# Optimization experiments

Measured on AMD Instinct MI355X. Metric: run time of the kernel, lower is better.

Reference implementation:

```python
import jax, jax.numpy as jnp
import numpy as np
import math

B, S, E, NH = 1024, 16, 32, 4  # batch, seq, attn embed dim, heads
H = 64                          # lstm1 hidden; lstm2 hidden = H//2 = E


def _pos_encoding(s, d):
    pos = jnp.arange(s, dtype=jnp.float32)[:, None]
    div = jnp.exp(jnp.arange(0, d, 2, dtype=jnp.float32) * (-math.log(10000.0) / d))
    pe = jnp.zeros((s, d), jnp.float32)
    pe = pe.at[:, 0::2].set(jnp.sin(pos * div))
    pe = pe.at[:, 1::2].set(jnp.cos(pos * div))
    return pe


def _lstm(x, wih, whh, bih, bhh):
    # x: [B,S,in]; PyTorch gate order i,f,g,o; h0=c0=0
    b = x.shape[0]
    h_dim = whh.shape[1]
    xg = jnp.einsum('bsi,gi->bsg', x, wih) + bih + bhh  # precompute input contribution

    def step(carry, xt):
        h, c = carry
        g = xt + h @ whh.T
        i, f, gg, o = jnp.split(g, 4, axis=-1)
        c = jax.nn.sigmoid(f) * c + jax.nn.sigmoid(i) * jnp.tanh(gg)
        h = jax.nn.sigmoid(o) * jnp.tanh(c)
        return (h, c), h

    h0 = jnp.zeros((b, h_dim), x.dtype)
    _, hs = jax.lax.scan(step, (h0, h0), jnp.swapaxes(xg, 0, 1))
    return jnp.swapaxes(hs, 0, 1)  # [B,S,H]


def setup_inputs() -> dict:
    key = jax.random.key(0)
    ks = jax.random.split(key, 24)

    def rn(k, shape, s=0.15):
        return jax.random.normal(k, shape, jnp.float32) * s

    return {
        'x': jax.random.normal(ks[0], (B, S, 1), jnp.float32),
        'emb_w': rn(ks[1], (32, 1)), 'emb_b': rn(ks[2], (32,), 0.05),
        'l1_wih': rn(ks[3], (4 * H, 32)), 'l1_whh': rn(ks[4], (4 * H, H)),
        'l1_bih': rn(ks[5], (4 * H,), 0.05), 'l1_bhh': rn(ks[6], (4 * H,), 0.05),
        'l2_wih': rn(ks[7], (4 * (H // 2), H)), 'l2_whh': rn(ks[8], (4 * (H // 2), H // 2)),
        'l2_bih': rn(ks[9], (4 * (H // 2),), 0.05), 'l2_bhh': rn(ks[10], (4 * (H // 2),), 0.05),
        'attn_w': rn(ks[11], (3 * E, E)), 'attn_b': rn(ks[12], (3 * E,), 0.05),
        'attn_ow': rn(ks[13], (E, E)), 'attn_ob': rn(ks[14], (E,), 0.05),
        'd1_w': rn(ks[15], (64, E)), 'd1_b': rn(ks[16], (64,), 0.05),
        'bn1_g': jnp.ones((64,), jnp.float32), 'bn1_b': jnp.zeros((64,), jnp.float32),
        'd2_w': rn(ks[17], (32, 64)), 'd2_b': rn(ks[18], (32,), 0.05),
        'bn2_g': jnp.ones((32,), jnp.float32), 'bn2_b': jnp.zeros((32,), jnp.float32),
        'd3_w': rn(ks[19], (1, 32)), 'd3_b': rn(ks[20], (1,), 0.05),
    }


def reference(x, emb_w, emb_b, l1_wih, l1_whh, l1_bih, l1_bhh,
              l2_wih, l2_whh, l2_bih, l2_bhh,
              attn_w, attn_b, attn_ow, attn_ob,
              d1_w, d1_b, bn1_g, bn1_b, d2_w, d2_b, bn2_g, bn2_b, d3_w, d3_b):
    eps = 1e-5
    h = x @ emb_w.T + emb_b                      # [B,S,32]
    h = h + _pos_encoding(h.shape[1], h.shape[2])
    l1 = _lstm(h, l1_wih, l1_whh, l1_bih, l1_bhh)          # [B,S,64]  (dropout: eval -> id)
    l2 = _lstm(l1, l2_wih, l2_whh, l2_bih, l2_bhh)         # [B,S,32]
    l2 = l2 + l1[:, :, :l2.shape[2]]                        # residual

    # nn.MultiheadAttention with default batch_first=False: attends over axis 0 (=B here),
    # faithful to the original module's behavior.
    L, N, _ = l2.shape
    hd = E // NH
    qkv = l2 @ attn_w.T + attn_b
    q, k, v = jnp.split(qkv, 3, axis=-1)
    q = q.reshape(L, N, NH, hd) * (1.0 / math.sqrt(hd))
    k = k.reshape(L, N, NH, hd)
    v = v.reshape(L, N, NH, hd)
    scores = jnp.einsum('lnhd,mnhd->nhlm', q, k)           # [S,4,B,B]
    a = jax.nn.softmax(scores, axis=-1)
    att = jnp.einsum('nhlm,mnhd->lnhd', a, v).reshape(L, N, E)
    att = att @ attn_ow.T + attn_ob

    z = att[:, -1, :]                                       # [B,32]

    def bn(t, g, b):  # eval-mode BatchNorm1d with fresh running stats (mean=0, var=1)
        return t * (g / jnp.sqrt(1.0 + eps)) + b

    z = jax.nn.relu(bn(z @ d1_w.T + d1_b, bn1_g, bn1_b))
    z = jax.nn.relu(bn(z @ d2_w.T + d2_b, bn2_g, bn2_b))
    return jax.nn.sigmoid(z @ d3_w.T + d3_b)                # [B,1]
```

## Files before the change

### kernel.cpp

```cpp
#include <hip/hip_runtime.h>
#include <math.h>


typedef __attribute__((ext_vector_type(8))) short short8v;
typedef __attribute__((ext_vector_type(4))) float f32x4;

__device__ __forceinline__ float sigf(float x) { return 1.0f / (1.0f + __expf(-x)); }
__device__ __forceinline__ float tanh_f(float x) {
    float a = fabsf(x);
    float e = __expf(2.0f * a);
    float t = 1.0f - 2.0f / (e + 1.0f);
    return copysignf(t, x);
}
__device__ __forceinline__ unsigned short f2bf(float f) {
    unsigned int u = __float_as_uint(f);
    unsigned int r = (u + 0x7FFFu + ((u >> 16) & 1u)) >> 16;
    return (unsigned short)r;
}

__global__ __launch_bounds__(256, 1) void lstm_kernel(
    const float* __restrict__ x,
    const float* __restrict__ emb_w, const float* __restrict__ emb_b,
    const float* __restrict__ wih1, const float* __restrict__ whh1,
    const float* __restrict__ bih1, const float* __restrict__ bhh1,
    const float* __restrict__ wih2, const float* __restrict__ whh2,
    const float* __restrict__ bih2, const float* __restrict__ bhh2,
    const float* __restrict__ attn_w, const float* __restrict__ attn_b,
    float* __restrict__ Q, float* __restrict__ K, float* __restrict__ V) {
    const int tid = threadIdx.x;
    const int w = tid >> 6, lane = tid & 63;
    const int l15 = lane & 15, q4 = lane >> 4;
    const int base = blockIdx.x * 16;

    __shared__ __align__(16) unsigned char E_raw[16 * 1024];
    __shared__ __align__(16) unsigned char H1_raw[2][2048];
    __shared__ __align__(16) unsigned char H2_raw[2][1024];
    __shared__ __align__(16) unsigned char WF2[24 * 1024];
    __shared__ __align__(16) float L1F[16][64];
    __shared__ __align__(16) float L2F[16][32];

    const unsigned jx7 = (unsigned)(l15 & 7) << 4;
    const unsigned jx4 = (unsigned)(l15 & 3) << 4;

    short8v w1f[4][3];
#pragma unroll
    for (int t = 0; t < 4; t++) {
        const int row = (w + 4 * t) * 16 + l15;
#pragma unroll
        for (int sl = 0; sl < 3; sl++) {
            short8v f;
#pragma unroll
            for (int e = 0; e < 8; e++) {
                int k = sl * 32 + q4 * 8 + e;
                float v = (k < 64) ? whh1[row * 64 + k] : wih1[row * 32 + (k - 64)];
                f[e] = (short)f2bf(v);
            }
            w1f[t][sl] = f;
        }
    }

    for (int f = w; f < 24; f += 4) {
        int t2 = f / 3, sl = f - t2 * 3;
        int row = t2 * 16 + l15;
        int koff = sl * 32 + q4 * 8;
        const float* src = (sl < 2) ? (wih2 + row * 64 + koff) : (whh2 + row * 32 + (koff - 64));
        float4 va = *(const float4*)(src);
        float4 vb = *(const float4*)(src + 4);
        short8v pk;
        pk[0] = (short)f2bf(va.x); pk[1] = (short)f2bf(va.y);
        pk[2] = (short)f2bf(va.z); pk[3] = (short)f2bf(va.w);
        pk[4] = (short)f2bf(vb.x); pk[5] = (short)f2bf(vb.y);
        pk[6] = (short)f2bf(vb.z); pk[7] = (short)f2bf(vb.w);
        *(short8v*)(&WF2[f * 1024 + lane * 16]) = pk;
    }

    float b1r[4][4];
#pragma unroll
    for (int t = 0; t < 4; t++)
#pragma unroll
        for (int e = 0; e < 4; e++) {
            int r = (w + 4 * t) * 16 + q4 * 4 + e;
            b1r[t][e] = bih1[r] + bhh1[r];
        }
    float b2r[4][4];
#pragma unroll
    for (int t = 0; t < 4; t++)
#pragma unroll
        for (int e = 0; e < 4; e++) {
            int r = ((w & 1) + 2 * t) * 16 + q4 * 4 + e;
            b2r[t][e] = bih2[r] + bhh2[r];
        }

    *(unsigned long long*)(H1_raw[0] + tid * 8) = 0ULL;
    if (tid < 128) *(unsigned long long*)(H2_raw[0] + tid * 8) = 0ULL;
    {
        const int je = tid >> 4, se = tid & 15;
        float xv = x[(base + je) * 16 + se];
        float ev[32];
#pragma unroll
        for (int ii = 0; ii < 16; ii++) {
            float d = __expf(-0.28782313662425574f * (float)(2 * ii));
            float ang = (float)se * d;
            ev[2 * ii] = xv * emb_w[2 * ii] + emb_b[2 * ii] + __sinf(ang);
            ev[2 * ii + 1] = xv * emb_w[2 * ii + 1] + emb_b[2 * ii + 1] + __cosf(ang);
        }
        unsigned jm = (unsigned)(je & 3) << 4;
#pragma unroll
        for (int b = 0; b < 4; b++) {
            short8v pk;
#pragma unroll
            for (int e = 0; e < 8; e++) pk[e] = (short)f2bf(ev[b * 8 + e]);
            *(short8v*)(&E_raw[se * 1024 + je * 64 + (((unsigned)(b * 16)) ^ jm)]) = pk;
        }
    }
    float c1[4] = {0.f, 0.f, 0.f, 0.f};
    float c2[4] = {0.f, 0.f, 0.f, 0.f};
    __syncthreads();

    const int u0 = w * 16 + q4 * 4;
    const int u20 = w * 16 + q4 * 4;

#define L2FRAG(T, SL) (*(const short8v*)(&WF2[(((w + 2 * (T)) * 3 + (SL)) << 10) + lane * 16]))

#pragma unroll 2
    for (int s = 0; s < 16; s++) {
        const int p = s & 1, pn = p ^ 1;
        const unsigned char* H1p = H1_raw[p];
        unsigned char* H1n = H1_raw[pn];
        short8v B0 = *(const short8v*)(H1p + (((unsigned)(l15 * 128 + q4 * 16)) ^ jx7));
        short8v B1 = *(const short8v*)(H1p + (((unsigned)(l15 * 128 + 64 + q4 * 16)) ^ jx7));
        short8v BE = *(const short8v*)(&E_raw[s * 1024] + (((unsigned)(l15 * 64 + q4 * 16)) ^ jx4));
        f32x4 a0 = {b1r[0][0], b1r[0][1], b1r[0][2], b1r[0][3]};
        f32x4 a1 = {b1r[1][0], b1r[1][1], b1r[1][2], b1r[1][3]};
        f32x4 a2 = {b1r[2][0], b1r[2][1], b1r[2][2], b1r[2][3]};
        f32x4 a3 = {b1r[3][0], b1r[3][1], b1r[3][2], b1r[3][3]};
        a0 = __builtin_amdgcn_mfma_f32_16x16x32_bf16(w1f[0][0], B0, a0, 0, 0, 0);
        a1 = __builtin_amdgcn_mfma_f32_16x16x32_bf16(w1f[1][0], B0, a1, 0, 0, 0);
        a2 = __builtin_amdgcn_mfma_f32_16x16x32_bf16(w1f[2][0], B0, a2, 0, 0, 0);
        a3 = __builtin_amdgcn_mfma_f32_16x16x32_bf16(w1f[3][0], B0, a3, 0, 0, 0);
        a0 = __builtin_amdgcn_mfma_f32_16x16x32_bf16(w1f[0][1], B1, a0, 0, 0, 0);
        a1 = __builtin_amdgcn_mfma_f32_16x16x32_bf16(w1f[1][1], B1, a1, 0, 0, 0);
        a2 = __builtin_amdgcn_mfma_f32_16x16x32_bf16(w1f[2][1], B1, a2, 0, 0, 0);
        a3 = __builtin_amdgcn_mfma_f32_16x16x32_bf16(w1f[3][1], B1, a3, 0, 0, 0);
        a0 = __builtin_amdgcn_mfma_f32_16x16x32_bf16(w1f[0][2], BE, a0, 0, 0, 0);
        a1 = __builtin_amdgcn_mfma_f32_16x16x32_bf16(w1f[1][2], BE, a1, 0, 0, 0);
        a2 = __builtin_amdgcn_mfma_f32_16x16x32_bf16(w1f[2][2], BE, a2, 0, 0, 0);
        a3 = __builtin_amdgcn_mfma_f32_16x16x32_bf16(w1f[3][2], BE, a3, 0, 0, 0);
        float h1v[4];
#pragma unroll
        for (int e = 0; e < 4; e++) {
            c1[e] = sigf(a1[e]) * c1[e] + sigf(a0[e]) * tanh_f(a2[e]);
            h1v[e] = sigf(a3[e]) * tanh_f(c1[e]);
        }
        {
            unsigned long long pk =
                (unsigned long long)f2bf(h1v[0]) | ((unsigned long long)f2bf(h1v[1]) << 16) |
                ((unsigned long long)f2bf(h1v[2]) << 32) | ((unsigned long long)f2bf(h1v[3]) << 48);
            *(unsigned long long*)(H1n + (((unsigned)(l15 * 128 + u0 * 2)) ^ jx7)) = pk;
        }
        if (s == 15) *(float4*)(&L1F[l15][u0]) = make_float4(h1v[0], h1v[1], h1v[2], h1v[3]);
        __syncthreads();
        if (w < 2) {
            const unsigned char* H2p = H2_raw[p];
            short8v C0 = *(const short8v*)(H1n + (((unsigned)(l15 * 128 + q4 * 16)) ^ jx7));
            short8v C1f = *(const short8v*)(H1n + (((unsigned)(l15 * 128 + 64 + q4 * 16)) ^ jx7));
            short8v C2 = *(const short8v*)(H2p + (((unsigned)(l15 * 64 + q4 * 16)) ^ jx4));
            f32x4 d0 = {b2r[0][0], b2r[0][1], b2r[0][2], b2r[0][3]};
            f32x4 d1 = {b2r[1][0], b2r[1][1], b2r[1][2], b2r[1][3]};
            f32x4 d2 = {b2r[2][0], b2r[2][1], b2r[2][2], b2r[2][3]};
            f32x4 d3 = {b2r[3][0], b2r[3][1], b2r[3][2], b2r[3][3]};
            d0 = __builtin_amdgcn_mfma_f32_16x16x32_bf16(L2FRAG(0, 0), C0, d0, 0, 0, 0);
            d1 = __builtin_amdgcn_mfma_f32_16x16x32_bf16(L2FRAG(1, 0), C0, d1, 0, 0, 0);
            d2 = __builtin_amdgcn_mfma_f32_16x16x32_bf16(L2FRAG(2, 0), C0, d2, 0, 0, 0);
            d3 = __builtin_amdgcn_mfma_f32_16x16x32_bf16(L2FRAG(3, 0), C0, d3, 0, 0, 0);
            d0 = __builtin_amdgcn_mfma_f32_16x16x32_bf16(L2FRAG(0, 1), C1f, d0, 0, 0, 0);
            d1 = __builtin_amdgcn_mfma_f32_16x16x32_bf16(L2FRAG(1, 1), C1f, d1, 0, 0, 0);
            d2 = __builtin_amdgcn_mfma_f32_16x16x32_bf16(L2FRAG(2, 1), C1f, d2, 0, 0, 0);
            d3 = __builtin_amdgcn_mfma_f32_16x16x32_bf16(L2FRAG(3, 1), C1f, d3, 0, 0, 0);
            d0 = __builtin_amdgcn_mfma_f32_16x16x32_bf16(L2FRAG(0, 2), C2, d0, 0, 0, 0);
            d1 = __builtin_amdgcn_mfma_f32_16x16x32_bf16(L2FRAG(1, 2), C2, d1, 0, 0, 0);
            d2 = __builtin_amdgcn_mfma_f32_16x16x32_bf16(L2FRAG(2, 2), C2, d2, 0, 0, 0);
            d3 = __builtin_amdgcn_mfma_f32_16x16x32_bf16(L2FRAG(3, 2), C2, d3, 0, 0, 0);
            float h2v[4];
#pragma unroll
            for (int e = 0; e < 4; e++) {
                c2[e] = sigf(d1[e]) * c2[e] + sigf(d0[e]) * tanh_f(d2[e]);
                h2v[e] = sigf(d3[e]) * tanh_f(c2[e]);
            }
            unsigned long long pk =
                (unsigned long long)f2bf(h2v[0]) | ((unsigned long long)f2bf(h2v[1]) << 16) |
                ((unsigned long long)f2bf(h2v[2]) << 32) | ((unsigned long long)f2bf(h2v[3]) << 48);
            *(unsigned long long*)(H2_raw[pn] + (((unsigned)(l15 * 64 + u20 * 2)) ^ jx4)) = pk;
            if (s == 15) *(float4*)(&L2F[l15][u20]) = make_float4(h2v[0], h2v[1], h2v[2], h2v[3]);
        }
        __syncthreads();
    }

    {
        const int j = tid >> 4, rb = tid & 15;
        const int gb = base + j;
        const float4* l1p = (const float4*)(&L1F[j][0]);
        const float4* l2p = (const float4*)(&L2F[j][0]);
#pragma unroll
        for (int rep = 0; rep < 6; rep++) {
            int row = rb + 16 * rep;
            float acc = attn_b[row];
            const float4* wrow = (const float4*)(attn_w + row * 32);
#pragma unroll
            for (int k4 = 0; k4 < 8; k4++) {
                float4 lv1 = l1p[k4];
                float4 lv2 = l2p[k4];
                float4 ww = wrow[k4];
                float lx = lv2.x + lv1.x, ly = lv2.y + lv1.y, lz = lv2.z + lv1.z, lw = lv2.w + lv1.w;
                acc += lx * ww.x + ly * ww.y + lz * ww.z + lw * ww.w;
            }
            if (row < 32) Q[gb * 32 + row] = acc * 0.35355339059327373f;
            else if (row < 64) K[gb * 32 + (row - 32)] = acc;
            else V[gb * 32 + (row - 64)] = acc;
        }
    }
#undef L2FRAG
}

__global__ __launch_bounds__(256, 2) void attn_kernel(
    const float* __restrict__ Q, const float* __restrict__ K, const float* __restrict__ V,
    float* __restrict__ pm, float* __restrict__ ps, float* __restrict__ pacc) {
    int c = blockIdx.x & 15, lt = blockIdx.x >> 4;
    int t = threadIdx.x;
    int h = t >> 6, l = lt * 64 + (t & 63);
    __shared__ __align__(16) float Ks[64 * 32];
    __shared__ __align__(16) float Vs[64 * 32];
    {
        const float4* Kg = (const float4*)(K + c * 2048);
        const float4* Vg = (const float4*)(V + c * 2048);
        float4* K4 = (float4*)Ks;
        float4* V4 = (float4*)Vs;
        K4[t] = Kg[t];
        K4[t + 256] = Kg[t + 256];
        V4[t] = Vg[t];
        V4[t + 256] = Vg[t + 256];
    }
    const float4* qg = (const float4*)(Q + l * 32 + h * 8);
    float4 q0 = qg[0], q1 = qg[1];
    __syncthreads();
    float m_r = -1e30f, l_r = 0.f;
    float4 acc0 = {0, 0, 0, 0}, acc1 = {0, 0, 0, 0};
#pragma unroll 4
    for (int m = 0; m < 64; m++) {
        const float4* k4 = (const float4*)(Ks + m * 32 + h * 8);
        float4 ka = k4[0], kb = k4[1];
        float s = q0.x * ka.x + q0.y * ka.y + q0.z * ka.z + q0.w * ka.w +
                  q1.x * kb.x + q1.y * kb.y + q1.z * kb.z + q1.w * kb.w;
        const float4* v4 = (const float4*)(Vs + m * 32 + h * 8);
        float4 va = v4[0], vb = v4[1];
        float nm = fmaxf(m_r, s);
        float f = __expf(m_r - nm);
        float pp = __expf(s - nm);
        l_r = l_r * f + pp;
        acc0.x = acc0.x * f + pp * va.x;
        acc0.y = acc0.y * f + pp * va.y;
        acc0.z = acc0.z * f + pp * va.z;
        acc0.w = acc0.w * f + pp * va.w;
        acc1.x = acc1.x * f + pp * vb.x;
        acc1.y = acc1.y * f + pp * vb.y;
        acc1.z = acc1.z * f + pp * vb.z;
        acc1.w = acc1.w * f + pp * vb.w;
        m_r = nm;
    }
    int idx = (c * 4 + h) * 1024 + l;
    pm[idx] = m_r;
    ps[idx] = l_r;
    float4* po = (float4*)(pacc + idx * 8);
    po[0] = acc0;
    po[1] = acc1;
}

__global__ __launch_bounds__(256) void head_kernel(
    const float* __restrict__ pm, const float* __restrict__ ps, const float* __restrict__ pacc,
    const float* __restrict__ ow, const float* __restrict__ ob,
    const float* __restrict__ d1w, const float* __restrict__ d1b,
    const float* __restrict__ g1, const float* __restrict__ b1,
    const float* __restrict__ d2w, const float* __restrict__ d2b,
    const float* __restrict__ g2, const float* __restrict__ b2,
    const float* __restrict__ d3w, const float* __restrict__ d3b,
    float* __restrict__ out) {
    int wid = threadIdx.x >> 6, j = threadIdx.x & 63;
    int l = blockIdx.x * 4 + wid;
    __shared__ float att_s[4][32], z_s[4][32], r1s[4][64];
    if (j < 32) {
        int h = j >> 3, d = j & 7;
        float M = -1e30f;
#pragma unroll
        for (int c = 0; c < 16; c++) M = fmaxf(M, pm[(c * 4 + h) * 1024 + l]);
        float den = 0.f, num = 0.f;
#pragma unroll
        for (int c = 0; c < 16; c++) {
            int idx = (c * 4 + h) * 1024 + l;
            float e = __expf(pm[idx] - M);
            den += e * ps[idx];
            num += e * pacc[idx * 8 + d];
        }
        att_s[wid][j] = num / den;
    }
    __syncthreads();
    if (j < 32) {
        float a = ob[j];
#pragma unroll
        for (int i = 0; i < 32; i++) a += att_s[wid][i] * ow[j * 32 + i];
        z_s[wid][j] = a;
    }
    __syncthreads();
    const float inv = rsqrtf(1.0f + 1e-5f);
    if (j < 64) {
        float a = d1b[j];
#pragma unroll
        for (int i = 0; i < 32; i++) a += z_s[wid][i] * d1w[j * 32 + i];
        a = a * (g1[j] * inv) + b1[j];
        r1s[wid][j] = fmaxf(a, 0.f);
    }
    __syncthreads();
    if (j < 32) {
        float a = d2b[j];
#pragma unroll
        for (int i = 0; i < 64; i++) a += r1s[wid][i] * d2w[j * 64 + i];
        a = a * (g2[j] * inv) + b2[j];
        float r2 = fmaxf(a, 0.f);
        float p = r2 * d3w[j];
        p += __shfl_down(p, 16);
        p += __shfl_down(p, 8);
        p += __shfl_down(p, 4);
        p += __shfl_down(p, 2);
        p += __shfl_down(p, 1);
        if (j == 0) out[l] = 1.0f / (1.0f + __expf(-(p + d3b[0])));
    }
}

extern "C" void kernel_launch(void* const* d_in, const int* in_sizes, int n_in,
                              void* d_out, int out_size, void* d_ws, size_t ws_size,
                              hipStream_t stream) {
    const float* x      = (const float*)d_in[0];
    const float* emb_w  = (const float*)d_in[1];
    const float* emb_b  = (const float*)d_in[2];
    const float* l1_wih = (const float*)d_in[3];
    const float* l1_whh = (const float*)d_in[4];
    const float* l1_bih = (const float*)d_in[5];
    const float* l1_bhh = (const float*)d_in[6];
    const float* l2_wih = (const float*)d_in[7];
    const float* l2_whh = (const float*)d_in[8];
    const float* l2_bih = (const float*)d_in[9];
    const float* l2_bhh = (const float*)d_in[10];
    const float* attn_w = (const float*)d_in[11];
    const float* attn_b = (const float*)d_in[12];
    const float* attn_ow = (const float*)d_in[13];
    const float* attn_ob = (const float*)d_in[14];
    const float* d1_w  = (const float*)d_in[15];
    const float* d1_b  = (const float*)d_in[16];
    const float* bn1_g = (const float*)d_in[17];
    const float* bn1_b = (const float*)d_in[18];
    const float* d2_w  = (const float*)d_in[19];
    const float* d2_b  = (const float*)d_in[20];
    const float* bn2_g = (const float*)d_in[21];
    const float* bn2_b = (const float*)d_in[22];
    const float* d3_w  = (const float*)d_in[23];
    const float* d3_b  = (const float*)d_in[24];
    float* out = (float*)d_out;

    float* ws   = (float*)d_ws;
    float* Q    = ws;
    float* K    = ws + 32768;
    float* V    = ws + 65536;
    float* pm   = ws + 98304;
    float* ps   = ws + 163840;
    float* pacc = ws + 229376;

    lstm_kernel<<<64, 256, 0, stream>>>(x, emb_w, emb_b, l1_wih, l1_whh, l1_bih, l1_bhh,
                                        l2_wih, l2_whh, l2_bih, l2_bhh,
                                        attn_w, attn_b, Q, K, V);
    attn_kernel<<<256, 256, 0, stream>>>(Q, K, V, pm, ps, pacc);
    head_kernel<<<256, 256, 0, stream>>>(pm, ps, pacc, attn_ow, attn_ob, d1_w, d1_b,
                                         bn1_g, bn1_b, d2_w, d2_b, bn2_g, bn2_b,
                                         d3_w, d3_b, out);
}
```

Before: 162.5 us.

## Software-pipeline LSTM layers to halve barriers per step and use fast rcp/bf16 packing

Restructures the LSTM recurrence so layer-1 step s+1 runs after layer-2 step s within the same barrier interval. The two layers now share the H1 fragment loads, and the second __syncthreads per timestep goes away. The sigmoid and tanh divisions become hardware reciprocals, and bf16 packing uses v_cvt_pk_bf16_f32. The dense head loops in the attention-combine kernel are vectorized with float4. Risks are small precision differences from the approximate reciprocal and subtle correctness issues in the reordered double-buffer indexing.

```diff
diff --git a/kernel.cpp b/kernel.cpp
--- a/kernel.cpp
+++ b/kernel.cpp
@@ -5,17 +5,25 @@
 typedef __attribute__((ext_vector_type(8))) short short8v;
 typedef __attribute__((ext_vector_type(4))) float f32x4;
 
-__device__ __forceinline__ float sigf(float x) { return 1.0f / (1.0f + __expf(-x)); }
+__device__ __forceinline__ float sigf(float x) {
+    float e = __expf(-x);
+    return __builtin_amdgcn_rcpf(1.0f + e);
+}
 __device__ __forceinline__ float tanh_f(float x) {
     float a = fabsf(x);
     float e = __expf(2.0f * a);
-    float t = 1.0f - 2.0f / (e + 1.0f);
+    float t = 1.0f - 2.0f * __builtin_amdgcn_rcpf(e + 1.0f);
     return copysignf(t, x);
 }
 __device__ __forceinline__ unsigned short f2bf(float f) {
     unsigned int u = __float_as_uint(f);
     unsigned int r = (u + 0x7FFFu + ((u >> 16) & 1u)) >> 16;
     return (unsigned short)r;
+}
+__device__ __forceinline__ unsigned cvtpk_bf16(float lo, float hi) {
+    unsigned r;
+    asm("v_cvt_pk_bf16_f32 %0, %1, %2" : "=v"(r) : "v"(lo), "v"(hi));
+    return r;
 }
 
 __global__ __launch_bounds__(256, 1) void lstm_kernel(
@@ -91,8 +99,8 @@
             b2r[t][e] = bih2[r] + bhh2[r];
         }
 
-    *(unsigned long long*)(H1_raw[0] + tid * 8) = 0ULL;
-    if (tid < 128) *(unsigned long long*)(H2_raw[0] + tid * 8) = 0ULL;
+    *(unsigned long long*)(H1_raw[1] + tid * 8) = 0ULL;
+    if (tid < 128) *(unsigned long long*)(H2_raw[1] + tid * 8) = 0ULL;
     {
         const int je = tid >> 4, se = tid & 15;
         float xv = x[(base + je) * 16 + se];
@@ -115,25 +123,24 @@
     }
     float c1[4] = {0.f, 0.f, 0.f, 0.f};
     float c2[4] = {0.f, 0.f, 0.f, 0.f};
-    __syncthreads();
 
     const int u0 = w * 16 + q4 * 4;
-    const int u20 = w * 16 + q4 * 4;
-
+
+#define LDBE(S)  (*(const short8v*)(&E_raw[(S) * 1024] + (((unsigned)(l15 * 64 + q4 * 16)) ^ jx4)))
+#define LDB0(HP) (*(const short8v*)((HP) + (((unsigned)(l15 * 128 + q4 * 16)) ^ jx7)))
+#define LDB1(HP) (*(const short8v*)((HP) + (((unsigned)(l15 * 128 + 64 + q4 * 16)) ^ jx7)))
+#define LDC2(HP) (*(const short8v*)((HP) + (((unsigned)(l15 * 64 + q4 * 16)) ^ jx4)))
 #define L2FRAG(T, SL) (*(const short8v*)(&WF2[(((w + 2 * (T)) * 3 + (SL)) << 10) + lane * 16]))
 
-#pragma unroll 2
-    for (int s = 0; s < 16; s++) {
-        const int p = s & 1, pn = p ^ 1;
-        const unsigned char* H1p = H1_raw[p];
-        unsigned char* H1n = H1_raw[pn];
-        short8v B0 = *(const short8v*)(H1p + (((unsigned)(l15 * 128 + q4 * 16)) ^ jx7));
-        short8v B1 = *(const short8v*)(H1p + (((unsigned)(l15 * 128 + 64 + q4 * 16)) ^ jx7));
-        short8v BE = *(const short8v*)(&E_raw[s * 1024] + (((unsigned)(l15 * 64 + q4 * 16)) ^ jx4));
+    auto phase1 = [&](unsigned char* H1n, short8v BE, short8v B0, short8v B1, bool last) {
         f32x4 a0 = {b1r[0][0], b1r[0][1], b1r[0][2], b1r[0][3]};
         f32x4 a1 = {b1r[1][0], b1r[1][1], b1r[1][2], b1r[1][3]};
         f32x4 a2 = {b1r[2][0], b1r[2][1], b1r[2][2], b1r[2][3]};
         f32x4 a3 = {b1r[3][0], b1r[3][1], b1r[3][2], b1r[3][3]};
+        a0 = __builtin_amdgcn_mfma_f32_16x16x32_bf16(w1f[0][2], BE, a0, 0, 0, 0);
+        a1 = __builtin_amdgcn_mfma_f32_16x16x32_bf16(w1f[1][2], BE, a1, 0, 0, 0);
+        a2 = __builtin_amdgcn_mfma_f32_16x16x32_bf16(w1f[2][2], BE, a2, 0, 0, 0);
+        a3 = __builtin_amdgcn_mfma_f32_16x16x32_bf16(w1f[3][2], BE, a3, 0, 0, 0);
         a0 = __builtin_amdgcn_mfma_f32_16x16x32_bf16(w1f[0][0], B0, a0, 0, 0, 0);
         a1 = __builtin_amdgcn_mfma_f32_16x16x32_bf16(w1f[1][0], B0, a1, 0, 0, 0);
         a2 = __builtin_amdgcn_mfma_f32_16x16x32_bf16(w1f[2][0], B0, a2, 0, 0, 0);
@@ -142,41 +149,41 @@
         a1 = __builtin_amdgcn_mfma_f32_16x16x32_bf16(w1f[1][1], B1, a1, 0, 0, 0);
         a2 = __builtin_amdgcn_mfma_f32_16x16x32_bf16(w1f[2][1], B1, a2, 0, 0, 0);
         a3 = __builtin_amdgcn_mfma_f32_16x16x32_bf16(w1f[3][1], B1, a3, 0, 0, 0);
-        a0 = __builtin_amdgcn_mfma_f32_16x16x32_bf16(w1f[0][2], BE, a0, 0, 0, 0);
-        a1 = __builtin_amdgcn_mfma_f32_16x16x32_bf16(w1f[1][2], BE, a1, 0, 0, 0);
-        a2 = __builtin_amdgcn_mfma_f32_16x16x32_bf16(w1f[2][2], BE, a2, 0, 0, 0);
-        a3 = __builtin_amdgcn_mfma_f32_16x16x32_bf16(w1f[3][2], BE, a3, 0, 0, 0);
         float h1v[4];
 #pragma unroll
         for (int e = 0; e < 4; e++) {
             c1[e] = sigf(a1[e]) * c1[e] + sigf(a0[e]) * tanh_f(a2[e]);
             h1v[e] = sigf(a3[e]) * tanh_f(c1[e]);
         }
-        {
-            unsigned long long pk =
-                (unsigned long long)f2bf(h1v[0]) | ((unsigned long long)f2bf(h1v[1]) << 16) |
-                ((unsigned long long)f2bf(h1v[2]) << 32) | ((unsigned long long)f2bf(h1v[3]) << 48);
-            *(unsigned long long*)(H1n + (((unsigned)(l15 * 128 + u0 * 2)) ^ jx7)) = pk;
-        }
-        if (s == 15) *(float4*)(&L1F[l15][u0]) = make_float4(h1v[0], h1v[1], h1v[2], h1v[3]);
+        uint2 pk = make_uint2(cvtpk_bf16(h1v[0], h1v[1]), cvtpk_bf16(h1v[2], h1v[3]));
+        *(uint2*)(H1n + (((unsigned)(l15 * 128 + u0 * 2)) ^ jx7)) = pk;
+        if (last) *(float4*)(&L1F[l15][u0]) = make_float4(h1v[0], h1v[1], h1v[2], h1v[3]);
+    };
+
+    __syncthreads();
+    phase1(H1_raw[0], LDBE(0), LDB0(H1_raw[1]), LDB1(H1_raw[1]), false);
+
+#pragma unroll 2
+    for (int s = 0; s < 16; s++) {
+        const int p = s & 1;
         __syncthreads();
+        short8v BEn = LDBE((s < 15) ? (s + 1) : 15);
+        short8v B0 = LDB0(H1_raw[p]);
+        short8v B1 = LDB1(H1_raw[p]);
         if (w < 2) {
-            const unsigned char* H2p = H2_raw[p];
-            short8v C0 = *(const short8v*)(H1n + (((unsigned)(l15 * 128 + q4 * 16)) ^ jx7));
-            short8v C1f = *(const short8v*)(H1n + (((unsigned)(l15 * 128 + 64 + q4 * 16)) ^ jx7));
-            short8v C2 = *(const short8v*)(H2p + (((unsigned)(l15 * 64 + q4 * 16)) ^ jx4));
+            short8v C2 = LDC2(H2_raw[p ^ 1]);
             f32x4 d0 = {b2r[0][0], b2r[0][1], b2r[0][2], b2r[0][3]};
             f32x4 d1 = {b2r[1][0], b2r[1][1], b2r[1][2], b2r[1][3]};
             f32x4 d2 = {b2r[2][0], b2r[2][1], b2r[2][2], b2r[2][3]};
             f32x4 d3 = {b2r[3][0], b2r[3][1], b2r[3][2], b2r[3][3]};
-            d0 = __builtin_amdgcn_mfma_f32_16x16x32_bf16(L2FRAG(0, 0), C0, d0, 0, 0, 0);
-            d1 = __builtin_amdgcn_mfma_f32_16x16x32_bf16(L2FRAG(1, 0), C0, d1, 0, 0, 0);
-            d2 = __builtin_amdgcn_mfma_f32_16x16x32_bf16(L2FRAG(2, 0), C0, d2, 0, 0, 0);
-            d3 = __builtin_amdgcn_mfma_f32_16x16x32_bf16(L2FRAG(3, 0), C0, d3, 0, 0, 0);
-            d0 = __builtin_amdgcn_mfma_f32_16x16x32_bf16(L2FRAG(0, 1), C1f, d0, 0, 0, 0);
-            d1 = __builtin_amdgcn_mfma_f32_16x16x32_bf16(L2FRAG(1, 1), C1f, d1, 0, 0, 0);
-            d2 = __builtin_amdgcn_mfma_f32_16x16x32_bf16(L2FRAG(2, 1), C1f, d2, 0, 0, 0);
-            d3 = __builtin_amdgcn_mfma_f32_16x16x32_bf16(L2FRAG(3, 1), C1f, d3, 0, 0, 0);
+            d0 = __builtin_amdgcn_mfma_f32_16x16x32_bf16(L2FRAG(0, 0), B0, d0, 0, 0, 0);
+            d1 = __builtin_amdgcn_mfma_f32_16x16x32_bf16(L2FRAG(1, 0), B0, d1, 0, 0, 0);
+            d2 = __builtin_amdgcn_mfma_f32_16x16x32_bf16(L2FRAG(2, 0), B0, d2, 0, 0, 0);
+            d3 = __builtin_amdgcn_mfma_f32_16x16x32_bf16(L2FRAG(3, 0), B0, d3, 0, 0, 0);
+            d0 = __builtin_amdgcn_mfma_f32_16x16x32_bf16(L2FRAG(0, 1), B1, d0, 0, 0, 0);
+            d1 = __builtin_amdgcn_mfma_f32_16x16x32_bf16(L2FRAG(1, 1), B1, d1, 0, 0, 0);
+            d2 = __builtin_amdgcn_mfma_f32_16x16x32_bf16(L2FRAG(2, 1), B1, d2, 0, 0, 0);
+            d3 = __builtin_amdgcn_mfma_f32_16x16x32_bf16(L2FRAG(3, 1), B1, d3, 0, 0, 0);
             d0 = __builtin_amdgcn_mfma_f32_16x16x32_bf16(L2FRAG(0, 2), C2, d0, 0, 0, 0);
             d1 = __builtin_amdgcn_mfma_f32_16x16x32_bf16(L2FRAG(1, 2), C2, d1, 0, 0, 0);
             d2 = __builtin_amdgcn_mfma_f32_16x16x32_bf16(L2FRAG(2, 2), C2, d2, 0, 0, 0);
@@ -187,15 +194,14 @@
                 c2[e] = sigf(d1[e]) * c2[e] + sigf(d0[e]) * tanh_f(d2[e]);
                 h2v[e] = sigf(d3[e]) * tanh_f(c2[e]);
             }
-            unsigned long long pk =
-                (unsigned long long)f2bf(h2v[0]) | ((unsigned long long)f2bf(h2v[1]) << 16) |
-                ((unsigned long long)f2bf(h2v[2]) << 32) | ((unsigned long long)f2bf(h2v[3]) << 48);
-            *(unsigned long long*)(H2_raw[pn] + (((unsigned)(l15 * 64 + u20 * 2)) ^ jx4)) = pk;
-            if (s == 15) *(float4*)(&L2F[l15][u20]) = make_float4(h2v[0], h2v[1], h2v[2], h2v[3]);
-        }
-        __syncthreads();
-    }
-
+            uint2 pk = make_uint2(cvtpk_bf16(h2v[0], h2v[1]), cvtpk_bf16(h2v[2], h2v[3]));
+            *(uint2*)(H2_raw[p] + (((unsigned)(l15 * 64 + u0 * 2)) ^ jx4)) = pk;
+            if (s == 15) *(float4*)(&L2F[l15][u0]) = make_float4(h2v[0], h2v[1], h2v[2], h2v[3]);
+        }
+        if (s < 15) phase1(H1_raw[p ^ 1], BEn, B0, B1, (s + 1) == 15);
+    }
+
+    __syncthreads();
     {
         const int j = tid >> 4, rb = tid & 15;
         const int gb = base + j;
@@ -219,6 +225,10 @@
             else V[gb * 32 + (row - 64)] = acc;
         }
     }
+#undef LDBE
+#undef LDB0
+#undef LDB1
+#undef LDC2
 #undef L2FRAG
 }
 
@@ -305,24 +315,39 @@
     __syncthreads();
     if (j < 32) {
         float a = ob[j];
-#pragma unroll
-        for (int i = 0; i < 32; i++) a += att_s[wid][i] * ow[j * 32 + i];
+        const float4* aw = (const float4*)(&att_s[wid][0]);
+        const float4* wr = (const float4*)(ow + j * 32);
+#pragma unroll
+        for (int k4 = 0; k4 < 8; k4++) {
+            float4 u = aw[k4], wv = wr[k4];
+            a += u.x * wv.x + u.y * wv.y + u.z * wv.z + u.w * wv.w;
+        }
         z_s[wid][j] = a;
     }
     __syncthreads();
     const float inv = rsqrtf(1.0f + 1e-5f);
-    if (j < 64) {
+    {
         float a = d1b[j];
-#pragma unroll
-        for (int i = 0; i < 32; i++) a += z_s[wid][i] * d1w[j * 32 + i];
+        const float4* zw = (const float4*)(&z_s[wid][0]);
+        const float4* wr = (const float4*)(d1w + j * 32);
+#pragma unroll
+        for (int k4 = 0; k4 < 8; k4++) {
+            float4 u = zw[k4], wv = wr[k4];
+            a += u.x * wv.x + u.y * wv.y + u.z * wv.z + u.w * wv.w;
+        }
         a = a * (g1[j] * inv) + b1[j];
         r1s[wid][j] = fmaxf(a, 0.f);
     }
     __syncthreads();
     if (j < 32) {
         float a = d2b[j];
-#pragma unroll
-        for (int i = 0; i < 64; i++) a += r1s[wid][i] * d2w[j * 64 + i];
+        const float4* rw = (const float4*)(&r1s[wid][0]);
+        const float4* wr = (const float4*)(d2w + j * 64);
+#pragma unroll
+        for (int k4 = 0; k4 < 16; k4++) {
+            float4 u = rw[k4], wv = wr[k4];
+            a += u.x * wv.x + u.y * wv.y + u.z * wv.z + u.w * wv.w;
+        }
         a = a * (g2[j] * inv) + b2[j];
         float r2 = fmaxf(a, 0.f);
         float p = r2 * d3w[j];
@@ -331,7 +356,7 @@
         p += __shfl_down(p, 4);
         p += __shfl_down(p, 2);
         p += __shfl_down(p, 1);
-        if (j == 0) out[l] = 1.0f / (1.0f + __expf(-(p + d3b[0])));
+        if (j == 0) out[l] = __builtin_amdgcn_rcpf(1.0f + __expf(-(p + d3b[0])));
     }
 }
 
```

Result: faster. 144.2 us (-11.3%).
